# Optimization experiments

Measured on AMD Instinct MI355X. Metric: run time of the kernel, lower is better.

The kernel has to match this reference:

```python
import jax, jax.numpy as jnp
import numpy as np

B, S, H, NH, PF, L, V = 8, 1024, 1024, 16, 4096, 6, 32000
HD = H // NH
STD = 0.02
NEG = -1e10


def setup_inputs() -> dict:
    key = jax.random.key(0)
    ks = jax.random.split(key, 12)
    inp = {
        "src": jax.random.randint(ks[0], (B, S), 0, V),
        "src_mask": jnp.ones((B, 1, 1, S), dtype=bool),
        "tok_emb": jax.random.normal(ks[1], (V, H), jnp.float32) * STD,
        "pos_emb": jax.random.normal(ks[2], (S, H), jnp.float32) * STD,
        "Wq": jax.random.normal(ks[3], (L, H, H), jnp.float32) * STD,
        "bq": jnp.zeros((L, H), jnp.float32),
        "Wk": jax.random.normal(ks[4], (L, H, H), jnp.float32) * STD,
        "bk": jnp.zeros((L, H), jnp.float32),
        "Wv": jax.random.normal(ks[5], (L, H, H), jnp.float32) * STD,
        "bv": jnp.zeros((L, H), jnp.float32),
        "Wo": jax.random.normal(ks[6], (L, H, H), jnp.float32) * STD,
        "bo": jnp.zeros((L, H), jnp.float32),
        "W1": jax.random.normal(ks[7], (L, H, PF), jnp.float32) * STD,
        "b1": jnp.zeros((L, PF), jnp.float32),
        "W2": jax.random.normal(ks[8], (L, PF, H), jnp.float32) * STD,
        "b2": jnp.zeros((L, H), jnp.float32),
        "ln1_g": jnp.ones((L, H), jnp.float32),
        "ln1_b": jnp.zeros((L, H), jnp.float32),
        "ln2_g": jnp.ones((L, H), jnp.float32),
        "ln2_b": jnp.zeros((L, H), jnp.float32),
    }
    return inp


def layer_norm(x, g, b, eps=1e-5):
    m = jnp.mean(x, axis=-1, keepdims=True)
    v = jnp.mean((x - m) ** 2, axis=-1, keepdims=True)
    return (x - m) * jax.lax.rsqrt(v + eps) * g + b


def reference(src, src_mask, tok_emb, pos_emb, Wq, bq, Wk, bk, Wv, bv, Wo, bo,
              W1, b1, W2, b2, ln1_g, ln1_b, ln2_g, ln2_b):
    # embedding * sqrt(hid_dim) + positional embedding (dropout = identity at eval)
    x = tok_emb[src] * jnp.sqrt(jnp.float32(H)) + pos_emb[None, :S]
    attn_scale = jnp.sqrt(jnp.float32(HD))
    for l in range(L):
        # multi-head self-attention
        q = (x @ Wq[l] + bq[l]).reshape(B, S, NH, HD).transpose(0, 2, 1, 3)
        k = (x @ Wk[l] + bk[l]).reshape(B, S, NH, HD).transpose(0, 2, 1, 3)
        v = (x @ Wv[l] + bv[l]).reshape(B, S, NH, HD).transpose(0, 2, 1, 3)
        energy = jnp.einsum('bhqd,bhkd->bhqk', q, k) / attn_scale  # [B,NH,S,S]
        energy = jnp.where(src_mask, energy, NEG)
        attn = jax.nn.softmax(energy, axis=-1)
        o = jnp.einsum('bhqk,bhkd->bhqd', attn, v)
        o = o.transpose(0, 2, 1, 3).reshape(B, S, H) @ Wo[l] + bo[l]
        x = layer_norm(x + o, ln1_g[l], ln1_b[l])
        # position-wise feedforward
        f = jax.nn.relu(x @ W1[l] + b1[l]) @ W2[l] + b2[l]
        x = layer_norm(x + f, ln2_g[l], ln2_b[l])
    return x
```

## Files before the change

kernel.cpp:

```cpp
#include <hip/hip_runtime.h>
#include <cstdint>
#include <cstddef>


#define DI __device__ __forceinline__

typedef __attribute__((ext_vector_type(8))) short short8;
typedef __attribute__((ext_vector_type(4))) short s16x4;
typedef __attribute__((ext_vector_type(4))) float f32x4;
typedef __attribute__((ext_vector_type(4))) unsigned u32x4;

static constexpr int H  = 1024;
static constexpr int S  = 1024;
static constexpr int BB = 8;
static constexpr int NH = 16;
static constexpr int PF = 4096;
static constexpr int M  = BB * S;
static constexpr int L  = 6;

DI short f2bf(float f) {
  unsigned u = __builtin_bit_cast(unsigned, f);
  u += 0x7fffu + ((u >> 16) & 1u);
  return (short)(u >> 16);
}

DI unsigned packbf(float a, float b) {
  return (__builtin_bit_cast(unsigned, a) >> 16) |
         (__builtin_bit_cast(unsigned, b) & 0xffff0000u);
}

DI void async16(void* lds, const void* g) {
  __builtin_amdgcn_global_load_lds(
      (const __attribute__((address_space(1))) unsigned*)g,
      (__attribute__((address_space(3))) unsigned*)lds, 16, 0, 0);
}

DI f32x4 mfma16(short8 a, short8 b, f32x4 c) {
  return __builtin_amdgcn_mfma_f32_16x16x32_bf16(a, b, c, 0, 0, 0);
}

__global__ __launch_bounds__(256) void embed_kernel(
    const int* __restrict__ src, const float* __restrict__ tok,
    const float* __restrict__ pos, float* __restrict__ xf,
    short* __restrict__ xb) {
  const int row = blockIdx.x;
  const int s = row & (S - 1);
  const int i0 = threadIdx.x << 2;
  const int v = src[row];
  const float4 te = *(const float4*)(tok + (size_t)v * H + i0);
  const float4 pe = *(const float4*)(pos + (size_t)s * H + i0);
  float o[4] = {te.x * 32.f + pe.x, te.y * 32.f + pe.y,
                te.z * 32.f + pe.z, te.w * 32.f + pe.w};
  *(float4*)(xf + (size_t)row * H + i0) = make_float4(o[0], o[1], o[2], o[3]);
  s16x4 pk;
  pk[0] = f2bf(o[0]); pk[1] = f2bf(o[1]); pk[2] = f2bf(o[2]); pk[3] = f2bf(o[3]);
  *(s16x4*)(xb + (size_t)row * H + i0) = pk;
}

__global__ __launch_bounds__(256) void wconv_kernel(
    const float* __restrict__ W, short* __restrict__ Wt, int K, int N) {
  __shared__ float tile[64][65];
  const int ntn = N >> 6;
  const int k0 = (blockIdx.x / ntn) << 6;
  const int n0 = (blockIdx.x % ntn) << 6;
  const int r4 = threadIdx.x >> 6, cc = threadIdx.x & 63;
#pragma unroll
  for (int i = 0; i < 16; i++) {
    const int r = (i << 2) + r4;
    tile[r][cc] = W[(size_t)(k0 + r) * N + n0 + cc];
  }
  __syncthreads();
#pragma unroll
  for (int i = 0; i < 16; i++) {
    const int n = (i << 2) + r4;
    Wt[(size_t)(n0 + n) * K + k0 + cc] = f2bf(tile[cc][n]);
  }
}

template <int MREP, int EPI>
__global__ __launch_bounds__(512, 2) void gemm256(
    const short* __restrict__ A, const short* __restrict__ Bt,
    const float* __restrict__ bias, void* __restrict__ out,
    const int N, const int K) {
  constexpr int WM = 16 / MREP;
  constexpr int WN = 8 / WM;
  constexpr int BN = WN * 64;
  constexpr int BLB = BN / 128;
  constexpr int LPH = 2 + BLB;
  constexpr int SLOT = (256 + BN) * 32 * 2;
  extern __shared__ char lds[];

  const int tid = threadIdx.x;
  const int w = tid >> 6, lane = tid & 63;
  const int g = lane >> 4, ci = lane & 15;
  const int wm = w / WN, wn = w % WN;

  const int nbn = N / BN;
  const int bid = (int)blockIdx.x;
  const int xcd = bid & 7, i = bid >> 3;
  const int bm = ((xcd & 3) << 3) | (i & 7);
  const int bn = (xcd >> 2) * (nbn >> 1) + (i >> 3);
  const int brow = bm << 8;
  const int bcol = bn * BN;

  const int srow = lane >> 2;
  const int schk = (lane & 3) ^ (srow & 3);
  const short* aS[2];
#pragma unroll
  for (int j = 0; j < 2; j++)
    aS[j] = A + (size_t)(brow + w * 16 + j * 128 + srow) * K + schk * 8;
  const short* bS[BLB];
#pragma unroll
  for (int j = 0; j < BLB; j++)
    bS[j] = Bt + (size_t)(bcol + w * 16 + j * 128 + srow) * K + schk * 8;

  const int aoff = (wm * (MREP * 16) + ci) * 64 + ((g ^ (ci & 3)) << 4);
  const int boff = (wn * 64 + ci) * 64 + ((g ^ (ci & 3)) << 4);

  auto stageP = [&](int hh, int part) {
    char* sa = lds + (hh & 3) * SLOT;
    char* sb = sa + 16384;
    const int ko = hh << 5;
    if constexpr (MREP == 8) {
      async16(sa + (w * 64 + part * 512) * 16, aS[part] + ko);
      async16(sb + (w * 64 + part * 512) * 16, bS[part] + ko);
    } else {
      async16(sa + (w * 64) * 16, aS[0] + ko);
      async16(sa + (w * 64 + 512) * 16, aS[1] + ko);
      async16(sb + (w * 64) * 16, bS[0] + ko);
    }
  };
  auto stageAll = [&](int hh) {
    if constexpr (MREP == 8) { stageP(hh, 0); stageP(hh, 1); }
    else stageP(hh, 0);
  };

  f32x4 acc[MREP][4];
#pragma unroll
  for (int a = 0; a < MREP; a++)
#pragma unroll
    for (int b = 0; b < 4; b++) acc[a][b] = f32x4{0.f, 0.f, 0.f, 0.f};

  stageAll(0); stageAll(1); stageAll(2);
  if constexpr (MREP == 8) asm volatile("s_waitcnt vmcnt(8)" ::: "memory");
  else                     asm volatile("s_waitcnt vmcnt(6)" ::: "memory");
  __builtin_amdgcn_sched_barrier(0);
  __builtin_amdgcn_s_barrier();

  const int nt2 = K >> 5;
  for (int h = 0; h < nt2; h++) {
    const char* la = lds + (h & 3) * SLOT;
    const char* lb = la + 16384;
    const bool pf = (h + 3 < nt2);
    short8 bfr[4], afr[4];
#pragma unroll
    for (int ni = 0; ni < 4; ni++)
      bfr[ni] = *(const short8*)(lb + boff + ni * 1024);
#pragma unroll
    for (int mi = 0; mi < 4; mi++)
      afr[mi] = *(const short8*)(la + aoff + mi * 1024);
    if (pf) stageP(h + 3, 0);
    __builtin_amdgcn_s_barrier();
    asm volatile("s_waitcnt lgkmcnt(0)" ::: "memory");
    __builtin_amdgcn_sched_barrier(0);
    __builtin_amdgcn_s_setprio(1);
#pragma unroll
    for (int mi = 0; mi < 4; mi++)
#pragma unroll
      for (int ni = 0; ni < 4; ni++)
        acc[mi][ni] = mfma16(afr[mi], bfr[ni], acc[mi][ni]);
    __builtin_amdgcn_s_setprio(0);
    if constexpr (MREP == 8) {
      __builtin_amdgcn_s_barrier();
      short8 af2[4];
#pragma unroll
      for (int mi = 0; mi < 4; mi++)
        af2[mi] = *(const short8*)(la + aoff + (4 + mi) * 1024);
      if (pf) stageP(h + 3, 1);
      __builtin_amdgcn_s_barrier();
      asm volatile("s_waitcnt lgkmcnt(0)" ::: "memory");
      __builtin_amdgcn_sched_barrier(0);
      __builtin_amdgcn_s_setprio(1);
#pragma unroll
      for (int mi = 0; mi < 4; mi++)
#pragma unroll
        for (int ni = 0; ni < 4; ni++)
          acc[4 + mi][ni] = mfma16(af2[mi], bfr[ni], acc[4 + mi][ni]);
      __builtin_amdgcn_s_setprio(0);
    }
    if (h + 4 <= nt2) {
      if constexpr (MREP == 8) asm volatile("s_waitcnt vmcnt(8)" ::: "memory");
      else                     asm volatile("s_waitcnt vmcnt(6)" ::: "memory");
    } else if (h + 3 == nt2) {
      if constexpr (MREP == 8) asm volatile("s_waitcnt vmcnt(4)" ::: "memory");
      else                     asm volatile("s_waitcnt vmcnt(3)" ::: "memory");
    } else {
      asm volatile("s_waitcnt vmcnt(0)" ::: "memory");
    }
    __builtin_amdgcn_sched_barrier(0);
    __builtin_amdgcn_s_barrier();
  }

  if constexpr (EPI <= 2) {
#pragma unroll
    for (int mi = 0; mi < MREP; mi++) {
      float bv[4];
#pragma unroll
      for (int ni = 0; ni < 4; ni++)
        bv[ni] = bias[bcol + wn * 64 + ni * 16 + ci];
#pragma unroll
      for (int r = 0; r < 4; r++) {
        const int row = brow + wm * (MREP * 16) + mi * 16 + (g << 2) + r;
#pragma unroll
        for (int ni = 0; ni < 4; ni++) {
          const int col = bcol + wn * 64 + ni * 16 + ci;
          float vv = acc[mi][ni][r] + bv[ni];
          if constexpr (EPI == 1) vv = fmaxf(vv, 0.f);
          if constexpr (EPI == 2) ((float*)out)[(size_t)row * N + col] = vv;
          else ((short*)out)[(size_t)row * N + col] = f2bf(vv);
        }
      }
    }
  } else {
    __syncthreads();
    short* t = (short*)lds;
#pragma unroll
    for (int ni = 0; ni < 4; ni++) {
      const int d = wn * 64 + ni * 16 + ci;
      const float bv = bias[bcol + d];
#pragma unroll
      for (int mi = 0; mi < 4; mi++) {
        const int s0 = wm * 64 + mi * 16 + (g << 2);
        s16x4 pk;
#pragma unroll
        for (int r = 0; r < 4; r++) pk[r] = f2bf(acc[mi][ni][r] + bv);
        *(s16x4*)(t + d * 264 + s0) = pk;
      }
    }
    __syncthreads();
    const int b = brow >> 10;
    short* o = (short*)out;
#pragma unroll
    for (int rr = 0; rr < 8; rr++) {
      const int c = tid + rr * 512;
      const int d = c >> 5, sc = c & 31;
      const short8 v = *(const short8*)(t + d * 264 + sc * 8);
      *(short8*)(o + ((size_t)b * H + bcol + d) * S + (brow & (S - 1)) + sc * 8) = v;
    }
  }
}

__global__ __launch_bounds__(256) void attn_kernel(
    const short* __restrict__ q, const short* __restrict__ k,
    const short* __restrict__ vt, short* __restrict__ ao) {
  __shared__ short lsk[2][4096];
  __shared__ short lsv[2][4096];
  const int tid = threadIdx.x;
  const int w = tid >> 6, lane = tid & 63;
  const int g = lane >> 4, ci = lane & 15;
  const int bid = ((int)blockIdx.x & 7) * 256 + ((int)blockIdx.x >> 3);
  const int qt = bid & 15;
  const int bh = bid >> 4;
  const int b = bh >> 4, h = bh & 15;
  const int hbase = h << 6;

  const int r8 = lane >> 3, c8 = lane & 7;
  const int cs = c8 ^ r8;
  const short* kbase = k + ((size_t)b * S) * H + hbase;
  const short* vbase = vt + ((size_t)b * H + hbase) * S;

  const size_t qrow = (size_t)b * S + (qt << 6) + (w << 4) + ci;
  short8 qf[2];
#pragma unroll
  for (int ks = 0; ks < 2; ks++)
    qf[ks] = *(const short8*)(q + qrow * H + hbase + ks * 32 + (g << 3));

  const int swz = ci & 7;
  int koff[2], voff[2][2];
#pragma unroll
  for (int ks = 0; ks < 2; ks++) {
    koff[ks] = ci * 128 + (((4 * ks + g) ^ swz) << 4);
#pragma unroll
    for (int pc = 0; pc < 2; pc++)
      voff[ks][pc] =
          ci * 128 + (((4 * ks + 2 * pc + (g >> 1)) ^ swz) << 4) + ((g & 1) << 3);
  }

#pragma unroll
  for (int t = 0; t < 2; t++) {
    const int row = (w << 3) + t * 32 + r8;
    async16(&lsk[0][t * 2048 + (w << 9)], kbase + (size_t)row * H + cs * 8);
    async16(&lsv[0][t * 2048 + (w << 9)], vbase + (size_t)row * S + cs * 8);
  }
  __syncthreads();

  const f32x4 zero = {0.f, 0.f, 0.f, 0.f};
  f32x4 of[4];
#pragma unroll
  for (int nf = 0; nf < 4; nf++) of[nf] = zero;
  float mrun = -INFINITY, lsum = 0.f;

#pragma unroll 2
  for (int kt = 0; kt < 16; kt++) {
    const int cur = kt & 1;
    if (kt < 15) {
      const int kr1 = (kt + 1) << 6;
#pragma unroll
      for (int t = 0; t < 2; t++) {
        const int row = (w << 3) + t * 32 + r8;
        async16(&lsk[cur ^ 1][t * 2048 + (w << 9)],
                kbase + (size_t)(kr1 + row) * H + cs * 8);
        async16(&lsv[cur ^ 1][t * 2048 + (w << 9)],
                vbase + (size_t)row * S + kr1 + cs * 8);
      }
    }
    const char* kb = (const char*)lsk[cur];
    const char* vb = (const char*)lsv[cur];

    f32x4 st[4];
#pragma unroll
    for (int mf = 0; mf < 4; mf++) st[mf] = zero;
#pragma unroll
    for (int ks = 0; ks < 2; ks++)
#pragma unroll
      for (int mf = 0; mf < 4; mf++) {
        const short8 kf = *(const short8*)(kb + koff[ks] + mf * 2048);
        st[mf] = mfma16(kf, qf[ks], st[mf]);
      }

    float tmax = -INFINITY;
#pragma unroll
    for (int mf = 0; mf < 4; mf++)
#pragma unroll
      for (int r = 0; r < 4; r++) tmax = fmaxf(tmax, st[mf][r]);
    tmax = fmaxf(tmax, __shfl_xor(tmax, 16));
    tmax = fmaxf(tmax, __shfl_xor(tmax, 32));
    const float mnew = fmaxf(mrun, tmax * 0.125f);
    const float alpha = __expf(mrun - mnew);
    float rs = 0.f;
    float p[4][4];
#pragma unroll
    for (int mf = 0; mf < 4; mf++)
#pragma unroll
      for (int r = 0; r < 4; r++) {
        p[mf][r] = __expf(__builtin_fmaf(st[mf][r], 0.125f, -mnew));
        rs += p[mf][r];
      }
    rs += __shfl_xor(rs, 16);
    rs += __shfl_xor(rs, 32);
    lsum = lsum * alpha + rs;
    mrun = mnew;

    unsigned pk[4][2];
#pragma unroll
    for (int mf = 0; mf < 4; mf++) {
      pk[mf][0] = packbf(p[mf][0], p[mf][1]);
      pk[mf][1] = packbf(p[mf][2], p[mf][3]);
    }
#pragma unroll
    for (int nf = 0; nf < 4; nf++)
#pragma unroll
      for (int r = 0; r < 4; r++) of[nf][r] *= alpha;

#pragma unroll
    for (int ks = 0; ks < 2; ks++) {
      u32x4 uu;
      uu[0] = pk[2 * ks][0];
      uu[1] = pk[2 * ks][1];
      uu[2] = pk[2 * ks + 1][0];
      uu[3] = pk[2 * ks + 1][1];
      const short8 pfrag = __builtin_bit_cast(short8, uu);
#pragma unroll
      for (int nf = 0; nf < 4; nf++) {
        union { short8 v8; s16x4 h[2]; } vv;
        vv.h[0] = *(const s16x4*)(vb + voff[ks][0] + nf * 2048);
        vv.h[1] = *(const s16x4*)(vb + voff[ks][1] + nf * 2048);
        of[nf] = mfma16(vv.v8, pfrag, of[nf]);
      }
    }
    __syncthreads();
  }

  const float inv = 1.f / lsum;
#pragma unroll
  for (int nf = 0; nf < 4; nf++) {
    s16x4 o4;
#pragma unroll
    for (int r = 0; r < 4; r++) o4[r] = f2bf(of[nf][r] * inv);
    *(s16x4*)(ao + qrow * H + hbase + (nf << 4) + (g << 2)) = o4;
  }
}

__global__ __launch_bounds__(256) void ln_kernel(
    const float* __restrict__ x, const float* __restrict__ t,
    const float* __restrict__ gm, const float* __restrict__ bt,
    float* __restrict__ yf, short* __restrict__ yb) {
  const int row = blockIdx.x;
  const int i0 = threadIdx.x << 2;
  const size_t base = (size_t)row * H + i0;
  const float4 a = *(const float4*)(x + base);
  const float4 bb = *(const float4*)(t + base);
  float v[4] = {a.x + bb.x, a.y + bb.y, a.z + bb.z, a.w + bb.w};
  float s = v[0] + v[1] + v[2] + v[3];
  float qq = v[0] * v[0] + v[1] * v[1] + v[2] * v[2] + v[3] * v[3];
#pragma unroll
  for (int off = 32; off; off >>= 1) {
    s += __shfl_down(s, off);
    qq += __shfl_down(qq, off);
  }
  __shared__ float red[8];
  const int w = threadIdx.x >> 6, lane = threadIdx.x & 63;
  if (lane == 0) { red[w] = s; red[4 + w] = qq; }
  __syncthreads();
  s = red[0] + red[1] + red[2] + red[3];
  qq = red[4] + red[5] + red[6] + red[7];
  const float mean = s * (1.f / H);
  float var = qq * (1.f / H) - mean * mean;
  var = fmaxf(var, 0.f);
  const float rstd = rsqrtf(var + 1e-5f);
  const float4 gv = *(const float4*)(gm + i0);
  const float4 bv = *(const float4*)(bt + i0);
  float y[4] = {(v[0] - mean) * rstd * gv.x + bv.x,
                (v[1] - mean) * rstd * gv.y + bv.y,
                (v[2] - mean) * rstd * gv.z + bv.z,
                (v[3] - mean) * rstd * gv.w + bv.w};
  *(float4*)(yf + base) = make_float4(y[0], y[1], y[2], y[3]);
  s16x4 pk;
  pk[0] = f2bf(y[0]); pk[1] = f2bf(y[1]); pk[2] = f2bf(y[2]); pk[3] = f2bf(y[3]);
  *(s16x4*)(yb + base) = pk;
}

extern "C" void kernel_launch(void* const* d_in, const int* in_sizes, int n_in,
                              void* d_out, int out_size, void* d_ws, size_t ws_size,
                              hipStream_t stream) {
  const int* src = (const int*)d_in[0];
  const float* tok = (const float*)d_in[2];
  const float* pos = (const float*)d_in[3];
  const float* Wq = (const float*)d_in[4];
  const float* bq = (const float*)d_in[5];
  const float* Wk = (const float*)d_in[6];
  const float* bk = (const float*)d_in[7];
  const float* Wv = (const float*)d_in[8];
  const float* bv = (const float*)d_in[9];
  const float* Wo = (const float*)d_in[10];
  const float* bo = (const float*)d_in[11];
  const float* W1 = (const float*)d_in[12];
  const float* b1 = (const float*)d_in[13];
  const float* W2 = (const float*)d_in[14];
  const float* b2 = (const float*)d_in[15];
  const float* g1 = (const float*)d_in[16];
  const float* be1 = (const float*)d_in[17];
  const float* g2 = (const float*)d_in[18];
  const float* be2 = (const float*)d_in[19];

  hipFuncSetAttribute(reinterpret_cast<const void*>(gemm256<8, 1>),
                      hipFuncAttributeMaxDynamicSharedMemorySize, 131072);
  hipFuncSetAttribute(reinterpret_cast<const void*>(gemm256<4, 0>),
                      hipFuncAttributeMaxDynamicSharedMemorySize, 98304);
  hipFuncSetAttribute(reinterpret_cast<const void*>(gemm256<4, 2>),
                      hipFuncAttributeMaxDynamicSharedMemorySize, 98304);
  hipFuncSetAttribute(reinterpret_cast<const void*>(gemm256<4, 3>),
                      hipFuncAttributeMaxDynamicSharedMemorySize, 98304);

  char* p = (char*)d_ws;
  auto take = [&](size_t bytes) {
    char* r = p;
    p += (bytes + 255) & ~(size_t)255;
    return r;
  };
  float* xf   = (float*)take((size_t)M * H * 4);
  short* xb   = (short*)take((size_t)M * H * 2);
  float* tmp  = (float*)take((size_t)M * H * 4);
  short* qb   = (short*)take((size_t)M * H * 2);
  short* kbuf = (short*)take((size_t)M * H * 2);
  short* vtb  = (short*)take((size_t)M * H * 2);
  short* aob  = (short*)take((size_t)M * H * 2);
  short* fb   = (short*)take((size_t)M * PF * 2);
  short* wtq  = (short*)take((size_t)H * H * 2);
  short* wtk  = (short*)take((size_t)H * H * 2);
  short* wtv  = (short*)take((size_t)H * H * 2);
  short* wto  = (short*)take((size_t)H * H * 2);
  short* wt1  = (short*)take((size_t)H * PF * 2);
  short* wt2  = (short*)take((size_t)H * PF * 2);

  embed_kernel<<<M, 256, 0, stream>>>(src, tok, pos, xf, xb);

  for (int l = 0; l < L; l++) {
    wconv_kernel<<<(H / 64) * (H / 64), 256, 0, stream>>>(Wq + (size_t)l * H * H, wtq, H, H);
    wconv_kernel<<<(H / 64) * (H / 64), 256, 0, stream>>>(Wk + (size_t)l * H * H, wtk, H, H);
    wconv_kernel<<<(H / 64) * (H / 64), 256, 0, stream>>>(Wv + (size_t)l * H * H, wtv, H, H);
    wconv_kernel<<<(H / 64) * (H / 64), 256, 0, stream>>>(Wo + (size_t)l * H * H, wto, H, H);
    wconv_kernel<<<(H / 64) * (PF / 64), 256, 0, stream>>>(W1 + (size_t)l * H * PF, wt1, H, PF);
    wconv_kernel<<<(PF / 64) * (H / 64), 256, 0, stream>>>(W2 + (size_t)l * PF * H, wt2, PF, H);

    gemm256<4, 0><<<256, 512, 98304, stream>>>(xb, wtq, bq + (size_t)l * H, qb, H, H);
    gemm256<4, 0><<<256, 512, 98304, stream>>>(xb, wtk, bk + (size_t)l * H, kbuf, H, H);
    gemm256<4, 3><<<256, 512, 98304, stream>>>(xb, wtv, bv + (size_t)l * H, vtb, H, H);
    attn_kernel<<<BB * NH * (S / 64), 256, 0, stream>>>(qb, kbuf, vtb, aob);
    gemm256<4, 2><<<256, 512, 98304, stream>>>(aob, wto, bo + (size_t)l * H, tmp, H, H);
    ln_kernel<<<M, 256, 0, stream>>>(xf, tmp, g1 + (size_t)l * H, be1 + (size_t)l * H, xf, xb);
    gemm256<8, 1><<<512, 512, 131072, stream>>>(xb, wt1, b1 + (size_t)l * PF, fb, PF, H);
    gemm256<4, 2><<<256, 512, 98304, stream>>>(fb, wt2, b2 + (size_t)l * H, tmp, H, PF);
    float* yf = (l == L - 1) ? (float*)d_out : xf;
    ln_kernel<<<M, 256, 0, stream>>>(xf, tmp, g2 + (size_t)l * H, be2 + (size_t)l * H, yf, xb);
  }
}
```

Baseline: 2.326 ms.

## Rework GEMM pipeline to double-buffered 64-wide K tiles with 8-phase loads

Replaces the 4-slot, 32-wide K ring buffer in the bf16 GEMM with two buffers of 64-wide K tiles. Each tile is split into four phases, and each phase issues one slice of the next tile's async loads while MFMAs run on the current one. Fragment reuse also changes: the 256x128 variant now keeps A fragments across two phases and alternates B halves. The goal is fewer barriers and waitcnt stalls per unit of K. In exchange the prefetch distance is shorter (one tile ahead instead of three), which risks exposing memory latency.

```diff
diff --git a/kernel.cpp b/kernel.cpp
--- a/kernel.cpp
+++ b/kernel.cpp
@@ -77,144 +77,169 @@
   }
 }
 
-template <int MREP, int EPI>
-__global__ __launch_bounds__(512, 2) void gemm256(
+template <int NW, int EPI>
+__global__ __launch_bounds__(512, 2) void gemm8p(
     const short* __restrict__ A, const short* __restrict__ Bt,
     const float* __restrict__ bias, void* __restrict__ out,
     const int N, const int K) {
-  constexpr int WM = 16 / MREP;
-  constexpr int WN = 8 / WM;
-  constexpr int BN = WN * 64;
-  constexpr int BLB = BN / 128;
-  constexpr int LPH = 2 + BLB;
-  constexpr int SLOT = (256 + BN) * 32 * 2;
+  constexpr int WAVES_N = NW;
+  constexpr int BN = NW * 64;
+  constexpr int BSZ = BN * 64;
+  constexpr int BUFSZ = 32768 + 2 * BSZ;
+  constexpr int MR = 2 * NW;
   extern __shared__ char lds[];
 
   const int tid = threadIdx.x;
   const int w = tid >> 6, lane = tid & 63;
   const int g = lane >> 4, ci = lane & 15;
-  const int wm = w / WN, wn = w % WN;
+  const int wm = w / WAVES_N, wn = w % WAVES_N;
 
   const int nbn = N / BN;
   const int bid = (int)blockIdx.x;
-  const int xcd = bid & 7, i = bid >> 3;
-  const int bm = ((xcd & 3) << 3) | (i & 7);
-  const int bn = (xcd >> 2) * (nbn >> 1) + (i >> 3);
+  const int xcd = bid & 7, ii = bid >> 3;
+  const int bm = ((xcd & 3) << 3) | (ii & 7);
+  const int bn = (xcd >> 2) * (nbn >> 1) + (ii >> 3);
   const int brow = bm << 8;
   const int bcol = bn * BN;
 
   const int srow = lane >> 2;
-  const int schk = (lane & 3) ^ (srow & 3);
-  const short* aS[2];
+  const int schk = ((lane & 3) ^ (srow & 3)) << 3;
+  const short* aSrc[2];
 #pragma unroll
   for (int j = 0; j < 2; j++)
-    aS[j] = A + (size_t)(brow + w * 16 + j * 128 + srow) * K + schk * 8;
-  const short* bS[BLB];
-#pragma unroll
-  for (int j = 0; j < BLB; j++)
-    bS[j] = Bt + (size_t)(bcol + w * 16 + j * 128 + srow) * K + schk * 8;
-
-  const int aoff = (wm * (MREP * 16) + ci) * 64 + ((g ^ (ci & 3)) << 4);
-  const int boff = (wn * 64 + ci) * 64 + ((g ^ (ci & 3)) << 4);
-
-  auto stageP = [&](int hh, int part) {
-    char* sa = lds + (hh & 3) * SLOT;
-    char* sb = sa + 16384;
-    const int ko = hh << 5;
-    if constexpr (MREP == 8) {
-      async16(sa + (w * 64 + part * 512) * 16, aS[part] + ko);
-      async16(sb + (w * 64 + part * 512) * 16, bS[part] + ko);
+    aSrc[j] = A + (size_t)(brow + w * 16 + j * 128 + srow) * K + schk;
+  const short* bSrc[2];
+  if constexpr (NW == 4) {
+#pragma unroll
+    for (int j = 0; j < 2; j++)
+      bSrc[j] = Bt + (size_t)(bcol + w * 16 + j * 128 + srow) * K + schk;
+  } else {
+    bSrc[0] = Bt + (size_t)(bcol + (tid >> 2)) * K +
+              (((tid & 3) ^ ((tid >> 2) & 3)) << 3);
+    bSrc[1] = nullptr;
+  }
+
+  auto stageA = [&](int buf, int ks, int kg) {
+#pragma unroll
+    for (int j = 0; j < 2; j++)
+      async16(lds + buf * BUFSZ + ks * 16384 + (w * 64 + j * 512) * 16,
+              aSrc[j] + kg + ks * 32);
+  };
+  auto stageB = [&](int buf, int ks, int kg) {
+    if constexpr (NW == 4) {
+#pragma unroll
+      for (int j = 0; j < 2; j++)
+        async16(lds + buf * BUFSZ + 32768 + ks * BSZ + (w * 64 + j * 512) * 16,
+                bSrc[j] + kg + ks * 32);
     } else {
-      async16(sa + (w * 64) * 16, aS[0] + ko);
-      async16(sa + (w * 64 + 512) * 16, aS[1] + ko);
-      async16(sb + (w * 64) * 16, bS[0] + ko);
+      async16(lds + buf * BUFSZ + 32768 + ks * BSZ + w * 1024,
+              bSrc[0] + kg + ks * 32);
     }
   };
-  auto stageAll = [&](int hh) {
-    if constexpr (MREP == 8) { stageP(hh, 0); stageP(hh, 1); }
-    else stageP(hh, 0);
-  };
-
-  f32x4 acc[MREP][4];
-#pragma unroll
-  for (int a = 0; a < MREP; a++)
+
+  const int cswz = ci * 64 + ((g ^ (ci & 3)) << 4);
+
+  f32x4 acc[MR][4];
+#pragma unroll
+  for (int a = 0; a < MR; a++)
 #pragma unroll
     for (int b = 0; b < 4; b++) acc[a][b] = f32x4{0.f, 0.f, 0.f, 0.f};
 
-  stageAll(0); stageAll(1); stageAll(2);
-  if constexpr (MREP == 8) asm volatile("s_waitcnt vmcnt(8)" ::: "memory");
-  else                     asm volatile("s_waitcnt vmcnt(6)" ::: "memory");
+  stageA(0, 0, 0); stageB(0, 0, 0); stageA(0, 1, 0); stageB(0, 1, 0);
+  if constexpr (NW == 4) asm volatile("s_waitcnt vmcnt(4)" ::: "memory");
+  else                   asm volatile("s_waitcnt vmcnt(3)" ::: "memory");
   __builtin_amdgcn_sched_barrier(0);
   __builtin_amdgcn_s_barrier();
 
-  const int nt2 = K >> 5;
-  for (int h = 0; h < nt2; h++) {
-    const char* la = lds + (h & 3) * SLOT;
-    const char* lb = la + 16384;
-    const bool pf = (h + 3 < nt2);
-    short8 bfr[4], afr[4];
-#pragma unroll
-    for (int ni = 0; ni < 4; ni++)
-      bfr[ni] = *(const short8*)(lb + boff + ni * 1024);
-#pragma unroll
-    for (int mi = 0; mi < 4; mi++)
-      afr[mi] = *(const short8*)(la + aoff + mi * 1024);
-    if (pf) stageP(h + 3, 0);
-    __builtin_amdgcn_s_barrier();
-    asm volatile("s_waitcnt lgkmcnt(0)" ::: "memory");
-    __builtin_amdgcn_sched_barrier(0);
-    __builtin_amdgcn_s_setprio(1);
-#pragma unroll
-    for (int mi = 0; mi < 4; mi++)
-#pragma unroll
-      for (int ni = 0; ni < 4; ni++)
-        acc[mi][ni] = mfma16(afr[mi], bfr[ni], acc[mi][ni]);
-    __builtin_amdgcn_s_setprio(0);
-    if constexpr (MREP == 8) {
-      __builtin_amdgcn_s_barrier();
-      short8 af2[4];
-#pragma unroll
-      for (int mi = 0; mi < 4; mi++)
-        af2[mi] = *(const short8*)(la + aoff + (4 + mi) * 1024);
-      if (pf) stageP(h + 3, 1);
+  const int nt = K >> 6;
+  short8 afr[4], bfr[4];
+  for (int t = 0; t < nt; t++) {
+    const char* cb = lds + (t & 1) * BUFSZ;
+    const int nb = (t & 1) ^ 1;
+    const bool pf = (t + 1 < nt);
+    const int kg = (t + 1) << 6;
+#pragma unroll
+    for (int p = 0; p < 4; p++) {
+      const int ks = p >> 1, h = p & 1;
+      if constexpr (NW == 4) {
+        if (h == 0) {
+#pragma unroll
+          for (int nj = 0; nj < 4; nj++)
+            bfr[nj] = *(const short8*)(cb + 32768 + ks * BSZ + wn * 4096 +
+                                       nj * 1024 + cswz);
+        }
+#pragma unroll
+        for (int mi = 0; mi < 4; mi++)
+          afr[mi] = *(const short8*)(cb + ks * 16384 + wm * 8192 + h * 4096 +
+                                     mi * 1024 + cswz);
+      } else {
+        if (h == 0) {
+#pragma unroll
+          for (int mi = 0; mi < 4; mi++)
+            afr[mi] = *(const short8*)(cb + ks * 16384 + wm * 4096 +
+                                       mi * 1024 + cswz);
+        }
+#pragma unroll
+        for (int nj = 0; nj < 2; nj++)
+          bfr[nj] = *(const short8*)(cb + 32768 + ks * BSZ + wn * 4096 +
+                                     h * 2048 + nj * 1024 + cswz);
+      }
+      if (pf) {
+        if (p == 0) stageA(nb, 0, kg);
+        else if (p == 1) stageB(nb, 0, kg);
+        else if (p == 2) stageA(nb, 1, kg);
+        else stageB(nb, 1, kg);
+      }
       __builtin_amdgcn_s_barrier();
       asm volatile("s_waitcnt lgkmcnt(0)" ::: "memory");
       __builtin_amdgcn_sched_barrier(0);
       __builtin_amdgcn_s_setprio(1);
-#pragma unroll
-      for (int mi = 0; mi < 4; mi++)
-#pragma unroll
-        for (int ni = 0; ni < 4; ni++)
-          acc[4 + mi][ni] = mfma16(af2[mi], bfr[ni], acc[4 + mi][ni]);
+      if constexpr (NW == 4) {
+#pragma unroll
+        for (int mi = 0; mi < 4; mi++)
+#pragma unroll
+          for (int nj = 0; nj < 4; nj++)
+            acc[h * 4 + mi][nj] = mfma16(afr[mi], bfr[nj], acc[h * 4 + mi][nj]);
+      } else {
+#pragma unroll
+        for (int mi = 0; mi < 4; mi++)
+#pragma unroll
+          for (int nj = 0; nj < 2; nj++)
+            acc[mi][h * 2 + nj] = mfma16(afr[mi], bfr[nj], acc[mi][h * 2 + nj]);
+      }
       __builtin_amdgcn_s_setprio(0);
-    }
-    if (h + 4 <= nt2) {
-      if constexpr (MREP == 8) asm volatile("s_waitcnt vmcnt(8)" ::: "memory");
-      else                     asm volatile("s_waitcnt vmcnt(6)" ::: "memory");
-    } else if (h + 3 == nt2) {
-      if constexpr (MREP == 8) asm volatile("s_waitcnt vmcnt(4)" ::: "memory");
-      else                     asm volatile("s_waitcnt vmcnt(3)" ::: "memory");
-    } else {
-      asm volatile("s_waitcnt vmcnt(0)" ::: "memory");
-    }
-    __builtin_amdgcn_sched_barrier(0);
-    __builtin_amdgcn_s_barrier();
+      if (p == 1) {
+        if (pf) {
+          if constexpr (NW == 4) asm volatile("s_waitcnt vmcnt(4)" ::: "memory");
+          else                   asm volatile("s_waitcnt vmcnt(3)" ::: "memory");
+        } else {
+          asm volatile("s_waitcnt vmcnt(0)" ::: "memory");
+        }
+        __builtin_amdgcn_sched_barrier(0);
+      }
+      if (p == 3 && pf) {
+        if constexpr (NW == 4) asm volatile("s_waitcnt vmcnt(4)" ::: "memory");
+        else                   asm volatile("s_waitcnt vmcnt(3)" ::: "memory");
+        __builtin_amdgcn_sched_barrier(0);
+      }
+      __builtin_amdgcn_s_barrier();
+    }
   }
 
   if constexpr (EPI <= 2) {
 #pragma unroll
-    for (int mi = 0; mi < MREP; mi++) {
+    for (int mi = 0; mi < MR; mi++) {
       float bv[4];
 #pragma unroll
-      for (int ni = 0; ni < 4; ni++)
-        bv[ni] = bias[bcol + wn * 64 + ni * 16 + ci];
+      for (int nj = 0; nj < 4; nj++)
+        bv[nj] = bias[bcol + wn * 64 + nj * 16 + ci];
 #pragma unroll
       for (int r = 0; r < 4; r++) {
-        const int row = brow + wm * (MREP * 16) + mi * 16 + (g << 2) + r;
-#pragma unroll
-        for (int ni = 0; ni < 4; ni++) {
-          const int col = bcol + wn * 64 + ni * 16 + ci;
-          float vv = acc[mi][ni][r] + bv[ni];
+        const int row = brow + wm * (MR * 16) + mi * 16 + (g << 2) + r;
+#pragma unroll
+        for (int nj = 0; nj < 4; nj++) {
+          const int col = bcol + wn * 64 + nj * 16 + ci;
+          float vv = acc[mi][nj][r] + bv[nj];
           if constexpr (EPI == 1) vv = fmaxf(vv, 0.f);
           if constexpr (EPI == 2) ((float*)out)[(size_t)row * N + col] = vv;
           else ((short*)out)[(size_t)row * N + col] = f2bf(vv);
@@ -225,15 +250,15 @@
     __syncthreads();
     short* t = (short*)lds;
 #pragma unroll
-    for (int ni = 0; ni < 4; ni++) {
-      const int d = wn * 64 + ni * 16 + ci;
+    for (int nj = 0; nj < 4; nj++) {
+      const int d = wn * 64 + nj * 16 + ci;
       const float bv = bias[bcol + d];
 #pragma unroll
       for (int mi = 0; mi < 4; mi++) {
         const int s0 = wm * 64 + mi * 16 + (g << 2);
         s16x4 pk;
 #pragma unroll
-        for (int r = 0; r < 4; r++) pk[r] = f2bf(acc[mi][ni][r] + bv);
+        for (int r = 0; r < 4; r++) pk[r] = f2bf(acc[mi][nj][r] + bv);
         *(s16x4*)(t + d * 264 + s0) = pk;
       }
     }
@@ -453,13 +478,13 @@
   const float* g2 = (const float*)d_in[18];
   const float* be2 = (const float*)d_in[19];
 
-  hipFuncSetAttribute(reinterpret_cast<const void*>(gemm256<8, 1>),
+  hipFuncSetAttribute(reinterpret_cast<const void*>(gemm8p<4, 1>),
                       hipFuncAttributeMaxDynamicSharedMemorySize, 131072);
-  hipFuncSetAttribute(reinterpret_cast<const void*>(gemm256<4, 0>),
+  hipFuncSetAttribute(reinterpret_cast<const void*>(gemm8p<2, 0>),
                       hipFuncAttributeMaxDynamicSharedMemorySize, 98304);
-  hipFuncSetAttribute(reinterpret_cast<const void*>(gemm256<4, 2>),
+  hipFuncSetAttribute(reinterpret_cast<const void*>(gemm8p<2, 2>),
                       hipFuncAttributeMaxDynamicSharedMemorySize, 98304);
-  hipFuncSetAttribute(reinterpret_cast<const void*>(gemm256<4, 3>),
+  hipFuncSetAttribute(reinterpret_cast<const void*>(gemm8p<2, 3>),
                       hipFuncAttributeMaxDynamicSharedMemorySize, 98304);
 
   char* p = (char*)d_ws;
@@ -493,14 +518,14 @@
     wconv_kernel<<<(H / 64) * (PF / 64), 256, 0, stream>>>(W1 + (size_t)l * H * PF, wt1, H, PF);
     wconv_kernel<<<(PF / 64) * (H / 64), 256, 0, stream>>>(W2 + (size_t)l * PF * H, wt2, PF, H);
 
-    gemm256<4, 0><<<256, 512, 98304, stream>>>(xb, wtq, bq + (size_t)l * H, qb, H, H);
-    gemm256<4, 0><<<256, 512, 98304, stream>>>(xb, wtk, bk + (size_t)l * H, kbuf, H, H);
-    gemm256<4, 3><<<256, 512, 98304, stream>>>(xb, wtv, bv + (size_t)l * H, vtb, H, H);
+    gemm8p<2, 0><<<256, 512, 98304, stream>>>(xb, wtq, bq + (size_t)l * H, qb, H, H);
+    gemm8p<2, 0><<<256, 512, 98304, stream>>>(xb, wtk, bk + (size_t)l * H, kbuf, H, H);
+    gemm8p<2, 3><<<256, 512, 98304, stream>>>(xb, wtv, bv + (size_t)l * H, vtb, H, H);
     attn_kernel<<<BB * NH * (S / 64), 256, 0, stream>>>(qb, kbuf, vtb, aob);
-    gemm256<4, 2><<<256, 512, 98304, stream>>>(aob, wto, bo + (size_t)l * H, tmp, H, H);
+    gemm8p<2, 2><<<256, 512, 98304, stream>>>(aob, wto, bo + (size_t)l * H, tmp, H, H);
     ln_kernel<<<M, 256, 0, stream>>>(xf, tmp, g1 + (size_t)l * H, be1 + (size_t)l * H, xf, xb);
-    gemm256<8, 1><<<512, 512, 131072, stream>>>(xb, wt1, b1 + (size_t)l * PF, fb, PF, H);
-    gemm256<4, 2><<<256, 512, 98304, stream>>>(fb, wt2, b2 + (size_t)l * H, tmp, H, PF);
+    gemm8p<4, 1><<<512, 512, 131072, stream>>>(xb, wt1, b1 + (size_t)l * PF, fb, PF, H);
+    gemm8p<2, 2><<<256, 512, 98304, stream>>>(fb, wt2, b2 + (size_t)l * H, tmp, H, PF);
     float* yf = (l == L - 1) ? (float*)d_out : xf;
     ln_kernel<<<M, 256, 0, stream>>>(xf, tmp, g2 + (size_t)l * H, be2 + (size_t)l * H, yf, xb);
   }
```

New measurement: 2.341 ms. About the same (+0.6%).
